# Kernel tuning notes

Measured on AMD Instinct MI355X. Metric: run time of the kernel, lower is better.

The kernel has to match this reference:

```python
import jax, jax.numpy as jnp
import numpy as np

D_MODEL = 1024
N_HEADS = 16
HEAD = D_MODEL // N_HEADS  # 64
D_FF = 4096
LN_EPS = 1e-5


def _layernorm(x, g, b):
    mu = jnp.mean(x, axis=-1, keepdims=True)
    var = jnp.mean(jnp.square(x - mu), axis=-1, keepdims=True)
    return (x - mu) * jax.lax.rsqrt(var + LN_EPS) * g + b


def _mha(q_in, k_in, v_in, Wq, Wk, Wv, bv, causal):
    # Wq/Wk/Wv: [H, d_model, head]; bv: [H, head] (value proj has bias, q/k do not)
    q = jnp.einsum('bsd,hde->bhse', q_in, Wq)
    k = jnp.einsum('btd,hde->bhte', k_in, Wk)
    v = jnp.einsum('btd,hde->bhte', v_in, Wv) + bv[None, :, None, :]
    scale = HEAD ** -0.5
    scores = jnp.einsum('bhse,bhte->bhst', q, k) * scale
    if causal:
        S, T = scores.shape[-2], scores.shape[-1]
        mask = jnp.tril(jnp.ones((S, T), dtype=bool))
        scores = jnp.where(mask, scores, -jnp.inf)
    p = jax.nn.softmax(scores, axis=-1)
    o = jnp.einsum('bhst,bhte->bhse', p, v)  # [B,H,S,head]
    B, H, S, E = o.shape
    return o.transpose(0, 2, 1, 3).reshape(B, S, H * E)  # concat heads in order


def setup_inputs() -> dict:
    key = jax.random.key(0)
    ks = jax.random.split(key, 20)
    B, S, T = 2, 2048, 2048
    sd = D_MODEL ** -0.5
    inp = {
        'input_tensor': jax.random.normal(ks[0], (B, S, D_MODEL), jnp.float32),
        'encoder_output': jax.random.normal(ks[1], (B, T, D_MODEL), jnp.float32),
        # masked self-attention params
        'Wq1': jax.random.normal(ks[2], (N_HEADS, D_MODEL, HEAD), jnp.float32) * sd,
        'Wk1': jax.random.normal(ks[3], (N_HEADS, D_MODEL, HEAD), jnp.float32) * sd,
        'Wv1': jax.random.normal(ks[4], (N_HEADS, D_MODEL, HEAD), jnp.float32) * sd,
        'bv1': jnp.zeros((N_HEADS, HEAD), jnp.float32),
        # cross-attention params
        'Wq2': jax.random.normal(ks[5], (N_HEADS, D_MODEL, HEAD), jnp.float32) * sd,
        'Wk2': jax.random.normal(ks[6], (N_HEADS, D_MODEL, HEAD), jnp.float32) * sd,
        'Wv2': jax.random.normal(ks[7], (N_HEADS, D_MODEL, HEAD), jnp.float32) * sd,
        'bv2': jnp.zeros((N_HEADS, HEAD), jnp.float32),
        # layernorms
        'g1': jnp.ones((D_MODEL,), jnp.float32), 'be1': jnp.zeros((D_MODEL,), jnp.float32),
        'g2': jnp.ones((D_MODEL,), jnp.float32), 'be2': jnp.zeros((D_MODEL,), jnp.float32),
        'g3': jnp.ones((D_MODEL,), jnp.float32), 'be3': jnp.zeros((D_MODEL,), jnp.float32),
        # FFN
        'Wf1': jax.random.normal(ks[8], (D_MODEL, D_FF), jnp.float32) * sd,
        'bf1': jnp.zeros((D_FF,), jnp.float32),
        'Wf2': jax.random.normal(ks[9], (D_FF, D_MODEL), jnp.float32) * (D_FF ** -0.5),
        'bf2': jnp.zeros((D_MODEL,), jnp.float32),
    }
    return inp


def reference(input_tensor, encoder_output, Wq1, Wk1, Wv1, bv1, Wq2, Wk2, Wv2, bv2,
              g1, be1, g2, be2, g3, be3, Wf1, bf1, Wf2, bf2):
    x = input_tensor
    # masked (causal) self-attention; dropout is identity in eval
    sa = _mha(x, x, x, Wq1, Wk1, Wv1, bv1, causal=True)
    x = _layernorm(sa + input_tensor, g1, be1)
    # cross-attention with encoder output (no mask)
    ca = _mha(x, encoder_output, encoder_output, Wq2, Wk2, Wv2, bv2, causal=False)
    x = _layernorm(x + ca, g2, be2)
    # FFN
    ffn = jax.nn.relu(x @ Wf1 + bf1) @ Wf2 + bf2
    x = _layernorm(x + ffn, g3, be3)
    return x
```

## Files before the change

### kernel.cpp

```cpp
#include <hip/hip_runtime.h>
#include <stdint.h>
#include <stddef.h>

typedef __attribute__((ext_vector_type(8))) short short8;
typedef __attribute__((ext_vector_type(4))) short short4_t;
typedef __attribute__((ext_vector_type(4))) float float4_t;
typedef __attribute__((ext_vector_type(4))) unsigned uint4_t;

#define DEV static __device__ __forceinline__

#define QSCALE 0.18033688011112042f

DEV short f2bf(float f) {
  unsigned u = __builtin_bit_cast(unsigned, f);
  u = (u + 0x7FFFu + ((u >> 16) & 1u)) >> 16;
  return (short)(unsigned short)u;
}

DEV void load_lds16(const short* g, short* l) {
  __builtin_amdgcn_global_load_lds((const __attribute__((address_space(1))) void*)g,
                                   (__attribute__((address_space(3))) void*)l,
                                   16, 0, 0);
}

__global__ __launch_bounds__(256) void transpose_cvt(const float* __restrict__ src,
                                                     short* __restrict__ dst,
                                                     int R, int C) {
  __shared__ float t[64][65];
  src += (size_t)blockIdx.z * R * C;
  dst += (size_t)blockIdx.z * R * C;
  const int tid = threadIdx.x;
  const int r0 = blockIdx.y * 64, c0 = blockIdx.x * 64;
#pragma unroll
  for (int i = 0; i < 16; i++) {
    int r = i * 4 + (tid >> 6);
    t[r][tid & 63] = src[(size_t)(r0 + r) * C + c0 + (tid & 63)];
  }
  __syncthreads();
#pragma unroll
  for (int i = 0; i < 16; i++) {
    int c = i * 4 + (tid >> 6);
    dst[(size_t)(c0 + c) * R + r0 + (tid & 63)] = f2bf(t[tid & 63][c]);
  }
}

struct Repack6 {
  const float* src[6];
  short* dst[6];
};
__global__ __launch_bounds__(256) void transpose_cvt6(Repack6 a) {
  __shared__ float t[64][65];
  const int mat = blockIdx.z >> 4;
  const int head = blockIdx.z & 15;
  const float* src = a.src[mat] + (size_t)head * 1024 * 64;
  short* dst = a.dst[mat] + (size_t)head * 64 * 1024;
  const int tid = threadIdx.x;
  const int r0 = blockIdx.y * 64;
#pragma unroll
  for (int i = 0; i < 16; i++) {
    int r = i * 4 + (tid >> 6);
    t[r][tid & 63] = src[(size_t)(r0 + r) * 64 + (tid & 63)];
  }
  __syncthreads();
#pragma unroll
  for (int i = 0; i < 16; i++) {
    int c = i * 4 + (tid >> 6);
    dst[(size_t)c * 1024 + r0 + (tid & 63)] = f2bf(t[tid & 63][c]);
  }
}

__global__ __launch_bounds__(256) void cvt_bf16_2(const float* __restrict__ inA,
                                                  short* __restrict__ outA,
                                                  const float* __restrict__ inB,
                                                  short* __restrict__ outB, int n4) {
  int i = blockIdx.x * 256 + threadIdx.x;
  const float* in = blockIdx.z ? inB : inA;
  short* out = blockIdx.z ? outB : outA;
  if (i < n4) {
    float4_t v = ((const float4_t*)in)[i];
    short4_t o;
    o.x = f2bf(v.x); o.y = f2bf(v.y); o.z = f2bf(v.z); o.w = f2bf(v.w);
    ((short4_t*)out)[i] = o;
  }
}

struct GemmArgs {
  const short* A;
  const short* Bt;
  int M, N, K;
  float* outf;
  short* outb;
  short* Qo;
  short* Ko;
  short* Vt;
  const float* bias;
};

template <int MODE>
DEV void scatter1(const GemmArgs& args, int row, int col, float v) {
  if constexpr (MODE == 0) {
    int sel = col >> 10, cc = col & 1023;
    int h = cc >> 6, e = cc & 63;
    int b_ = row >> 11, s = row & 2047;
    if (sel == 0)
      args.Qo[(((size_t)(b_ * 16 + h)) * 2048 + s) * 64 + e] = f2bf(v * QSCALE);
    else if (sel == 1)
      args.Ko[(((size_t)(b_ * 16 + h)) * 2048 + s) * 64 + e] = f2bf(v);
    else {
      v += args.bias[cc];
      args.Vt[(((size_t)(b_ * 16 + h)) * 64 + e) * 2048 + s] = f2bf(v);
    }
  } else if constexpr (MODE == 1) {
    int h = col >> 6, e = col & 63;
    int b_ = row >> 11, s = row & 2047;
    args.Qo[(((size_t)(b_ * 16 + h)) * 2048 + s) * 64 + e] = f2bf(v * QSCALE);
  } else if constexpr (MODE == 2) {
    int sel = col >> 10, cc = col & 1023;
    int h = cc >> 6, e = cc & 63;
    int b_ = row >> 11, s = row & 2047;
    if (sel == 0)
      args.Ko[(((size_t)(b_ * 16 + h)) * 2048 + s) * 64 + e] = f2bf(v);
    else {
      v += args.bias[cc];
      args.Vt[(((size_t)(b_ * 16 + h)) * 64 + e) * 2048 + s] = f2bf(v);
    }
  } else if constexpr (MODE == 3) {
    v += args.bias[col];
    v = v > 0.f ? v : 0.f;
    args.outb[(size_t)row * args.N + col] = f2bf(v);
  } else {
    v += args.bias[col];
    args.outf[(size_t)row * args.N + col] = v;
  }
}

template <int MODE>
__global__ __launch_bounds__(256) void gemm_k(GemmArgs args) {
  constexpr int BM = 128, BK = 64;
  __shared__ short As[2][BM * BK];
  __shared__ short Bs[2][BM * BK];
  const int tid = threadIdx.x;
  const int lane = tid & 63;
  const int w = tid >> 6;
  const int wr = w >> 1, wc = w & 1;

  const int nwgx = gridDim.x;
  const int nxy = nwgx * gridDim.y;
  const int nwg = nxy * gridDim.z;
  const int orig = (blockIdx.z * gridDim.y + blockIdx.y) * nwgx + blockIdx.x;
  const int q8 = nwg >> 3;
  const int swz = (orig & 7) * q8 + (orig >> 3);
  const int zsl = swz / nxy;
  const int xy = swz % nxy;
  const int row0 = (xy / nwgx) * BM;
  const int col0 = (xy % nwgx) * BM;

  const int K = args.K;
  const int kLen = K / gridDim.z;
  const int kbase = zsl * kLen;
  const short* Ab = args.A + (size_t)row0 * K;
  const short* Bb = args.Bt + (size_t)col0 * K;
  float4_t acc[4][4] = {};
  const int r = lane & 15, kg = lane >> 4, rx = r & 7;

  auto stage = [&](int buf, int k0) {
#pragma unroll
    for (int i = 0; i < 4; i++) {
      int c = i * 256 + tid;
      int rw = c >> 3, sc = (c & 7) ^ (rw & 7);
      load_lds16(Ab + (size_t)rw * K + k0 + sc * 8, &As[buf][c * 8]);
    }
#pragma unroll
    for (int i = 0; i < 4; i++) {
      int c = i * 256 + tid;
      int rw = c >> 3, sc = (c & 7) ^ (rw & 7);
      load_lds16(Bb + (size_t)rw * K + k0 + sc * 8, &Bs[buf][c * 8]);
    }
  };

  stage(0, kbase);
  __syncthreads();
  int buf = 0;
  const int nk = kLen / BK;
  for (int t = 0; t < nk; t++) {
    if (t + 1 < nk) stage(buf ^ 1, kbase + (t + 1) * BK);
#pragma unroll
    for (int kk = 0; kk < BK; kk += 32) {
      const int ch = kk >> 3;
      short8 a[4], b[4];
#pragma unroll
      for (int m = 0; m < 4; m++)
        a[m] = *(const short8*)&As[buf][(wr * 64 + m * 16 + r) * BK + ((ch + kg) ^ rx) * 8];
#pragma unroll
      for (int n = 0; n < 4; n++)
        b[n] = *(const short8*)&Bs[buf][(wc * 64 + n * 16 + r) * BK + ((ch + kg) ^ rx) * 8];
#pragma unroll
      for (int m = 0; m < 4; m++)
#pragma unroll
        for (int n = 0; n < 4; n++)
          acc[m][n] = __builtin_amdgcn_mfma_f32_16x16x32_bf16(a[m], b[n], acc[m][n], 0, 0, 0);
    }
    __syncthreads();
    buf ^= 1;
  }

  float* dst5 = args.outf + (size_t)zsl * args.M * args.N;
#pragma unroll
  for (int m = 0; m < 4; m++)
#pragma unroll
    for (int n = 0; n < 4; n++)
#pragma unroll
      for (int j = 0; j < 4; j++) {
        int row = row0 + wr * 64 + m * 16 + kg * 4 + j;
        int col = col0 + wc * 64 + n * 16 + r;
        if constexpr (MODE == 5)
          dst5[(size_t)row * args.N + col] = acc[m][n][j];
        else
          scatter1<MODE>(args, row, col, acc[m][n][j]);
      }
}

template <int MODE>
__global__ __launch_bounds__(512, 2) void gemm256_k(GemmArgs args) {
  extern __shared__ short lds[];
  const int tid = threadIdx.x;
  const int lane = tid & 63;
  const int w = tid >> 6;
  const int wr = w >> 2, wc = w & 3;

  const int nwgx = gridDim.x;
  const int nwg = nwgx * gridDim.y;
  const int orig = blockIdx.y * nwgx + blockIdx.x;
  const int q8 = nwg >> 3;
  const int swz = (orig & 7) * q8 + (orig >> 3);
  const int row0 = (swz / nwgx) * 256;
  const int col0 = (swz % nwgx) * 256;

  const int K = args.K;
  const short* Ab = args.A + (size_t)row0 * K;
  const short* Bb = args.Bt + (size_t)col0 * K;
  const int r = lane & 15, kg = lane >> 4, rx = r & 7;
  float4_t acc[8][4] = {};

  auto stage = [&](int buf, int k0) {
    short* Ad = lds + buf * 16384;
    short* Bd = lds + 32768 + buf * 16384;
#pragma unroll
    for (int i = 0; i < 4; i++) {
      int c = i * 512 + tid;
      int rw = c >> 3, sc = (c & 7) ^ (rw & 7);
      load_lds16(Ab + (size_t)rw * K + k0 + sc * 8, Ad + c * 8);
    }
#pragma unroll
    for (int i = 0; i < 4; i++) {
      int c = i * 512 + tid;
      int rw = c >> 3, sc = (c & 7) ^ (rw & 7);
      load_lds16(Bb + (size_t)rw * K + k0 + sc * 8, Bd + c * 8);
    }
  };

  stage(0, 0);
  __syncthreads();
  int buf = 0;
  const int nk = K / 64;
  for (int t = 0; t < nk; t++) {
    if (t + 1 < nk) stage(buf ^ 1, (t + 1) * 64);
    const short* Ar = lds + buf * 16384;
    const short* Br = lds + 32768 + buf * 16384;
#pragma unroll
    for (int kk = 0; kk < 64; kk += 32) {
      const int ch = kk >> 3;
      short8 a[8], b[4];
#pragma unroll
      for (int m = 0; m < 8; m++)
        a[m] = *(const short8*)&Ar[(wr * 128 + m * 16 + r) * 64 + ((ch + kg) ^ rx) * 8];
#pragma unroll
      for (int n = 0; n < 4; n++)
        b[n] = *(const short8*)&Br[(wc * 64 + n * 16 + r) * 64 + ((ch + kg) ^ rx) * 8];
#pragma unroll
      for (int m = 0; m < 8; m++)
#pragma unroll
        for (int n = 0; n < 4; n++)
          acc[m][n] = __builtin_amdgcn_mfma_f32_16x16x32_bf16(a[m], b[n], acc[m][n], 0, 0, 0);
    }
    __syncthreads();
    buf ^= 1;
  }

#pragma unroll
  for (int m = 0; m < 8; m++)
#pragma unroll
    for (int n = 0; n < 4; n++)
#pragma unroll
      for (int j = 0; j < 4; j++)
        scatter1<MODE>(args, row0 + wr * 128 + m * 16 + kg * 4 + j,
                       col0 + wc * 64 + n * 16 + r, acc[m][n][j]);
}

template <bool CAUSAL>
__global__ __launch_bounds__(256) void attn_k(const short* __restrict__ Q,
                                              const short* __restrict__ Kq,
                                              const short* __restrict__ Vt,
                                              float* __restrict__ Out) {
  __shared__ short kst[2][64 * 64];
  __shared__ short vst[2][64 * 64];
  __shared__ unsigned p_lds[4][16 * 32];
  const int tid = threadIdx.x;
  const int lane = tid & 63;
  const int w = tid >> 6;
  const int bh = blockIdx.y;
  const int b_ = bh >> 4, h = bh & 15;
  const int qt = (blockIdx.x + blockIdx.y) & (gridDim.x - 1);
  const int q0 = qt * 64 + w * 16;
  const int r = lane & 15, kg = lane >> 4;
  const int rx = r & 7;
  const size_t base = (size_t)bh * 2048 * 64;
  const short* Qb = Q + base;
  const short* Kb = Kq + base;
  const short* Vb = Vt + base;

  short8 q[2];
#pragma unroll
  for (int half = 0; half < 2; half++)
    q[half] = *(const short8*)&Qb[(size_t)(q0 + r) * 64 + half * 32 + kg * 8];

  float4_t o[4] = {};
  float lp = 0.f;

  const int NT = CAUSAL ? qt + 1 : 32;
  const float4_t zero4 = {0.f, 0.f, 0.f, 0.f};

  const int c0 = tid, c1 = tid + 256;
  const int row0s = c0 >> 3, cc0 = (c0 & 7) ^ (row0s & 7);
  const int row1s = c1 >> 3, cc1 = (c1 & 7) ^ (row1s & 7);

  auto stage = [&](int buf, int kt) {
    const short* ktk = Kb + (size_t)kt * 64 * 64;
    const short* ktv = Vb + (size_t)kt * 64;
    load_lds16(ktk + row0s * 64 + cc0 * 8, &kst[buf][c0 * 8]);
    load_lds16(ktk + row1s * 64 + cc1 * 8, &kst[buf][c1 * 8]);
    load_lds16(ktv + (size_t)row0s * 2048 + cc0 * 8, &vst[buf][c0 * 8]);
    load_lds16(ktv + (size_t)row1s * 2048 + cc1 * 8, &vst[buf][c1 * 8]);
  };

  stage(0, 0);
  __syncthreads();
  int buf = 0;

  for (int kt = 0; kt < NT; kt++) {
    if (kt + 1 < NT) stage(buf ^ 1, kt + 1);

    short8 kb[4][2];
#pragma unroll
    for (int grp = 0; grp < 4; grp++)
#pragma unroll
      for (int half = 0; half < 2; half++)
        kb[grp][half] = *(const short8*)&kst[buf][(grp * 16 + r) * 64 + ((half * 4 + kg) ^ rx) * 8];

    float4_t sc[4];
    __builtin_amdgcn_s_setprio(1);
#pragma unroll
    for (int grp = 0; grp < 4; grp++) {
      float4_t t0 = __builtin_amdgcn_mfma_f32_16x16x32_bf16(kb[grp][0], q[0], zero4, 0, 0, 0);
      sc[grp] = __builtin_amdgcn_mfma_f32_16x16x32_bf16(kb[grp][1], q[1], t0, 0, 0, 0);
    }
    __builtin_amdgcn_s_setprio(0);

    float s[16];
#pragma unroll
    for (int grp = 0; grp < 4; grp++)
#pragma unroll
      for (int j = 0; j < 4; j++) s[grp * 4 + j] = sc[grp][j];

    if (CAUSAL && kt == NT - 1) {
      const int qrow = q0 + r;
#pragma unroll
      for (int grp = 0; grp < 4; grp++)
#pragma unroll
        for (int j = 0; j < 4; j++)
          if (kt * 64 + grp * 16 + kg * 4 + j > qrow) s[grp * 4 + j] = -1e30f;
    }

    float p[16];
    float ps = 0.f;
#pragma unroll
    for (int i = 0; i < 16; i++) {
      p[i] = __builtin_amdgcn_exp2f(s[i]);
      ps += p[i];
    }
    lp += ps;

    unsigned* p32 = &p_lds[w][0];
#pragma unroll
    for (int grp = 0; grp < 4; grp++) {
      unsigned pk01, pk23;
      asm("v_cvt_pk_bf16_f32 %0, %1, %2" : "=v"(pk01) : "v"(p[grp * 4 + 0]), "v"(p[grp * 4 + 1]));
      asm("v_cvt_pk_bf16_f32 %0, %1, %2" : "=v"(pk23) : "v"(p[grp * 4 + 2]), "v"(p[grp * 4 + 3]));
      int idx = r * 32 + ((2 * grp + (kg >> 1)) ^ rx) * 4 + (kg & 1) * 2;
      p32[idx] = pk01;
      p32[idx + 1] = pk23;
    }
    __builtin_amdgcn_sched_barrier(0);

    short8 pa[2];
#pragma unroll
    for (int half = 0; half < 2; half++) {
      const int db = r * 32 + ((half * 4 + kg) ^ rx) * 4;
      uint4_t t;
      t.x = p32[db + 0];
      t.y = p32[db + 1];
      t.z = p32[db + 2];
      t.w = p32[db + 3];
      pa[half] = __builtin_bit_cast(short8, t);
    }

    __builtin_amdgcn_s_setprio(1);
#pragma unroll
    for (int n = 0; n < 4; n++) {
      short8 v0 = *(const short8*)&vst[buf][(n * 16 + r) * 64 + ((0 * 4 + kg) ^ rx) * 8];
      short8 v1 = *(const short8*)&vst[buf][(n * 16 + r) * 64 + ((1 * 4 + kg) ^ rx) * 8];
      o[n] = __builtin_amdgcn_mfma_f32_16x16x32_bf16(v0, pa[0], o[n], 0, 0, 0);
      o[n] = __builtin_amdgcn_mfma_f32_16x16x32_bf16(v1, pa[1], o[n], 0, 0, 0);
    }
    __builtin_amdgcn_s_setprio(0);

    __syncthreads();
    buf ^= 1;
  }

  lp += __shfl_xor(lp, 16);
  lp += __shfl_xor(lp, 32);
  const float inv = 1.0f / lp;
  float* orow = Out + ((size_t)b_ * 2048 + q0 + r) * 1024 + h * 64;
#pragma unroll
  for (int n = 0; n < 4; n++)
#pragma unroll
    for (int j = 0; j < 4; j++)
      orow[n * 16 + kg * 4 + j] = o[n][j] * inv;
}

__global__ __launch_bounds__(256) void add_ln_k(const float* __restrict__ X,
                                                const float* __restrict__ Y,
                                                const float* __restrict__ g,
                                                const float* __restrict__ be,
                                                float* __restrict__ outf,
                                                short* __restrict__ outb) {
  __shared__ float red[8];
  const int row = blockIdx.x;
  const int t = threadIdx.x;
  const int lane = t & 63, w = t >> 6;
  float4_t v = ((const float4_t*)(X + (size_t)row * 1024))[t];
  float4_t u = ((const float4_t*)(Y + (size_t)row * 1024))[t];
  v.x += u.x; v.y += u.y; v.z += u.z; v.w += u.w;
  float s = v.x + v.y + v.z + v.w;
#pragma unroll
  for (int off = 32; off >= 1; off >>= 1) s += __shfl_xor(s, off);
  if (lane == 0) red[w] = s;
  __syncthreads();
  float mean = (red[0] + red[1] + red[2] + red[3]) * (1.f / 1024.f);
  float dx = v.x - mean, dy = v.y - mean, dz = v.z - mean, dw = v.w - mean;
  float q2 = dx * dx + dy * dy + dz * dz + dw * dw;
#pragma unroll
  for (int off = 32; off >= 1; off >>= 1) q2 += __shfl_xor(q2, off);
  if (lane == 0) red[4 + w] = q2;
  __syncthreads();
  float var = (red[4] + red[5] + red[6] + red[7]) * (1.f / 1024.f);
  float rs = rsqrtf(var + 1e-5f);
  float4_t gg = ((const float4_t*)g)[t];
  float4_t bb = ((const float4_t*)be)[t];
  float4_t o;
  o.x = dx * rs * gg.x + bb.x;
  o.y = dy * rs * gg.y + bb.y;
  o.z = dz * rs * gg.z + bb.z;
  o.w = dw * rs * gg.w + bb.w;
  ((float4_t*)(outf + (size_t)row * 1024))[t] = o;
  if (outb != nullptr) {
    short4_t ob;
    ob.x = f2bf(o.x); ob.y = f2bf(o.y); ob.z = f2bf(o.z); ob.w = f2bf(o.w);
    ((short4_t*)(outb + (size_t)row * 1024))[t] = ob;
  }
}

__global__ __launch_bounds__(256) void add_ln2_k(const float* __restrict__ X,
                                                 const float* __restrict__ P0,
                                                 const float* __restrict__ P1,
                                                 const float* __restrict__ bias,
                                                 const float* __restrict__ g,
                                                 const float* __restrict__ be,
                                                 float* __restrict__ outf) {
  __shared__ float red[8];
  const int row = blockIdx.x;
  const int t = threadIdx.x;
  const int lane = t & 63, w = t >> 6;
  float4_t v = ((const float4_t*)(X + (size_t)row * 1024))[t];
  float4_t u0 = ((const float4_t*)(P0 + (size_t)row * 1024))[t];
  float4_t u1 = ((const float4_t*)(P1 + (size_t)row * 1024))[t];
  float4_t bi = ((const float4_t*)bias)[t];
  v.x += u0.x + u1.x + bi.x;
  v.y += u0.y + u1.y + bi.y;
  v.z += u0.z + u1.z + bi.z;
  v.w += u0.w + u1.w + bi.w;
  float s = v.x + v.y + v.z + v.w;
#pragma unroll
  for (int off = 32; off >= 1; off >>= 1) s += __shfl_xor(s, off);
  if (lane == 0) red[w] = s;
  __syncthreads();
  float mean = (red[0] + red[1] + red[2] + red[3]) * (1.f / 1024.f);
  float dx = v.x - mean, dy = v.y - mean, dz = v.z - mean, dw = v.w - mean;
  float q2 = dx * dx + dy * dy + dz * dz + dw * dw;
#pragma unroll
  for (int off = 32; off >= 1; off >>= 1) q2 += __shfl_xor(q2, off);
  if (lane == 0) red[4 + w] = q2;
  __syncthreads();
  float var = (red[4] + red[5] + red[6] + red[7]) * (1.f / 1024.f);
  float rs = rsqrtf(var + 1e-5f);
  float4_t gg = ((const float4_t*)g)[t];
  float4_t bb = ((const float4_t*)be)[t];
  float4_t o;
  o.x = dx * rs * gg.x + bb.x;
  o.y = dy * rs * gg.y + bb.y;
  o.z = dz * rs * gg.z + bb.z;
  o.w = dw * rs * gg.w + bb.w;
  ((float4_t*)(outf + (size_t)row * 1024))[t] = o;
}

extern "C" void kernel_launch(void* const* d_in, const int* in_sizes, int n_in,
                              void* d_out, int out_size, void* d_ws, size_t ws_size,
                              hipStream_t stream) {
  (void)in_sizes; (void)n_in; (void)out_size; (void)ws_size;
  const float* x_in = (const float*)d_in[0];
  const float* enc  = (const float*)d_in[1];
  const float* Wq1  = (const float*)d_in[2];
  const float* Wk1  = (const float*)d_in[3];
  const float* Wv1  = (const float*)d_in[4];
  const float* bv1  = (const float*)d_in[5];
  const float* Wq2  = (const float*)d_in[6];
  const float* Wk2  = (const float*)d_in[7];
  const float* Wv2  = (const float*)d_in[8];
  const float* bv2  = (const float*)d_in[9];
  const float* g1   = (const float*)d_in[10];
  const float* be1  = (const float*)d_in[11];
  const float* g2   = (const float*)d_in[12];
  const float* be2  = (const float*)d_in[13];
  const float* g3   = (const float*)d_in[14];
  const float* be3  = (const float*)d_in[15];
  const float* Wf1  = (const float*)d_in[16];
  const float* bf1  = (const float*)d_in[17];
  const float* Wf2  = (const float*)d_in[18];
  const float* bf2  = (const float*)d_in[19];
  float* out = (float*)d_out;

  (void)hipFuncSetAttribute((const void*)gemm256_k<0>,
                            hipFuncAttributeMaxDynamicSharedMemorySize, 131072);
  (void)hipFuncSetAttribute((const void*)gemm256_k<3>,
                            hipFuncAttributeMaxDynamicSharedMemorySize, 131072);

  char* ws = (char*)d_ws;
  size_t off = 0;
  auto alloc = [&](size_t bytes) -> void* {
    void* p = ws + off;
    off += (bytes + 255) & ~(size_t)255;
    return p;
  };
  short* wqkv1t = (short*)alloc((size_t)3072 * 1024 * 2);
  short* wq2t   = (short*)alloc((size_t)1024 * 1024 * 2);
  short* wkv2t  = (short*)alloc((size_t)2048 * 1024 * 2);
  short* wf1t   = (short*)alloc((size_t)4096 * 1024 * 2);
  short* wf2t   = (short*)alloc((size_t)1024 * 4096 * 2);
  short* act_bf = (short*)alloc((size_t)4096 * 1024 * 2);
  short* enc_bf = (short*)alloc((size_t)4096 * 1024 * 2);
  short* Qb     = (short*)alloc((size_t)4096 * 1024 * 2);
  short* Kb     = (short*)alloc((size_t)4096 * 1024 * 2);
  short* Vtb    = (short*)alloc((size_t)4096 * 1024 * 2);
  float* tmp_f  = (float*)alloc((size_t)4096 * 1024 * 4);
  float* xbuf   = (float*)alloc((size_t)4096 * 1024 * 4);
  short* h_bf   = (short*)alloc((size_t)4096 * 4096 * 2);
  float* pbuf   = (float*)alloc((size_t)2 * 4096 * 1024 * 4);

  dim3 blk(256);
  dim3 blk5(512);
  Repack6 rp;
  rp.src[0] = Wq1; rp.dst[0] = wqkv1t;
  rp.src[1] = Wk1; rp.dst[1] = wqkv1t + 1024 * 1024;
  rp.src[2] = Wv1; rp.dst[2] = wqkv1t + 2 * 1024 * 1024;
  rp.src[3] = Wq2; rp.dst[3] = wq2t;
  rp.src[4] = Wk2; rp.dst[4] = wkv2t;
  rp.src[5] = Wv2; rp.dst[5] = wkv2t + 1024 * 1024;
  transpose_cvt6<<<dim3(1, 16, 96), blk, 0, stream>>>(rp);
  transpose_cvt<<<dim3(64, 16, 1), blk, 0, stream>>>(Wf1, wf1t, 1024, 4096);
  transpose_cvt<<<dim3(16, 64, 1), blk, 0, stream>>>(Wf2, wf2t, 4096, 1024);
  cvt_bf16_2<<<dim3(4096, 1, 2), blk, 0, stream>>>(x_in, act_bf, enc, enc_bf, 1048576);

  GemmArgs ga;
  ga.A = act_bf; ga.Bt = wqkv1t; ga.M = 4096; ga.N = 3072; ga.K = 1024;
  ga.outf = nullptr; ga.outb = nullptr; ga.Qo = Qb; ga.Ko = Kb; ga.Vt = Vtb; ga.bias = bv1;
  gemm256_k<0><<<dim3(12, 16), blk5, 131072, stream>>>(ga);
  attn_k<true><<<dim3(32, 32), blk, 0, stream>>>(Qb, Kb, Vtb, tmp_f);
  add_ln_k<<<4096, blk, 0, stream>>>(tmp_f, x_in, g1, be1, xbuf, act_bf);

  ga.A = act_bf; ga.Bt = wq2t; ga.M = 4096; ga.N = 1024; ga.K = 1024;
  ga.Qo = Qb; ga.Ko = nullptr; ga.Vt = nullptr; ga.bias = nullptr;
  gemm_k<1><<<dim3(8, 32), blk, 0, stream>>>(ga);
  ga.A = enc_bf; ga.Bt = wkv2t; ga.M = 4096; ga.N = 2048; ga.K = 1024;
  ga.Qo = nullptr; ga.Ko = Kb; ga.Vt = Vtb; ga.bias = bv2;
  gemm_k<2><<<dim3(16, 32), blk, 0, stream>>>(ga);
  attn_k<false><<<dim3(32, 32), blk, 0, stream>>>(Qb, Kb, Vtb, tmp_f);
  add_ln_k<<<4096, blk, 0, stream>>>(xbuf, tmp_f, g2, be2, xbuf, act_bf);

  ga.A = act_bf; ga.Bt = wf1t; ga.M = 4096; ga.N = 4096; ga.K = 1024;
  ga.outb = h_bf; ga.bias = bf1; ga.Qo = nullptr; ga.Ko = nullptr; ga.Vt = nullptr;
  gemm256_k<3><<<dim3(16, 16), blk5, 131072, stream>>>(ga);
  ga.A = h_bf; ga.Bt = wf2t; ga.M = 4096; ga.N = 1024; ga.K = 4096;
  ga.outf = pbuf; ga.outb = nullptr; ga.bias = nullptr;
  gemm_k<5><<<dim3(8, 32, 2), blk, 0, stream>>>(ga);
  add_ln2_k<<<4096, blk, 0, stream>>>(xbuf, pbuf, pbuf + (size_t)4096 * 1024,
                                      bf2, g3, be3, out);
}
```

Baseline: 346.7 us.

## Merge cross-attention Q and KV projection GEMMs into one launch; unroll attention double-buffer

The separate Q-projection and KV-projection GEMMs for cross-attention are combined into a single grouped kernel that assigns the first 256 swizzled workgroups to the Q projection and the remaining 512 to the K/V projection. This cuts one launch and lets the two small GEMMs share the GPU instead of running back to back with tail underutilization. Separately, the attention loop is unrolled by two with compile-time buffer indices, so LDS addresses are constant and the runtime buffer toggle goes away. The risks are divergent scatter paths inside the fused kernel and more code size in the attention kernel.

```diff
diff --git a/kernel.cpp b/kernel.cpp
--- a/kernel.cpp
+++ b/kernel.cpp
@@ -1,6 +1,7 @@
 #include <hip/hip_runtime.h>
 #include <stdint.h>
 #include <stddef.h>
+#include <type_traits>
 
 typedef __attribute__((ext_vector_type(8))) short short8;
 typedef __attribute__((ext_vector_type(4))) short short4_t;
@@ -217,6 +218,86 @@
           dst5[(size_t)row * args.N + col] = acc[m][n][j];
         else
           scatter1<MODE>(args, row, col, acc[m][n][j]);
+      }
+}
+
+__global__ __launch_bounds__(256) void gemm_dual_k(GemmArgs a1, GemmArgs a2) {
+  constexpr int BM = 128, BK = 64;
+  __shared__ short As[2][BM * BK];
+  __shared__ short Bs[2][BM * BK];
+  const int tid = threadIdx.x;
+  const int lane = tid & 63;
+  const int w = tid >> 6;
+  const int wr = w >> 1, wc = w & 1;
+
+  const int nwg = gridDim.x;
+  const int orig = blockIdx.x;
+  const int q8 = nwg >> 3;
+  const int swz = (orig & 7) * q8 + (orig >> 3);
+  const bool isA = swz < 256;
+  const GemmArgs& args = isA ? a1 : a2;
+  const int id = isA ? swz : swz - 256;
+  const int ncols = isA ? 8 : 16;
+  const int row0 = (id / ncols) * BM;
+  const int col0 = (id % ncols) * BM;
+
+  const int K = 1024;
+  const short* Ab = args.A + (size_t)row0 * K;
+  const short* Bb = args.Bt + (size_t)col0 * K;
+  float4_t acc[4][4] = {};
+  const int r = lane & 15, kg = lane >> 4, rx = r & 7;
+
+  auto stage = [&](int buf, int k0) {
+#pragma unroll
+    for (int i = 0; i < 4; i++) {
+      int c = i * 256 + tid;
+      int rw = c >> 3, sc = (c & 7) ^ (rw & 7);
+      load_lds16(Ab + (size_t)rw * K + k0 + sc * 8, &As[buf][c * 8]);
+    }
+#pragma unroll
+    for (int i = 0; i < 4; i++) {
+      int c = i * 256 + tid;
+      int rw = c >> 3, sc = (c & 7) ^ (rw & 7);
+      load_lds16(Bb + (size_t)rw * K + k0 + sc * 8, &Bs[buf][c * 8]);
+    }
+  };
+
+  stage(0, 0);
+  __syncthreads();
+  int buf = 0;
+  const int nk = K / BK;
+  for (int t = 0; t < nk; t++) {
+    if (t + 1 < nk) stage(buf ^ 1, (t + 1) * BK);
+#pragma unroll
+    for (int kk = 0; kk < BK; kk += 32) {
+      const int ch = kk >> 3;
+      short8 a[4], b[4];
+#pragma unroll
+      for (int m = 0; m < 4; m++)
+        a[m] = *(const short8*)&As[buf][(wr * 64 + m * 16 + r) * BK + ((ch + kg) ^ rx) * 8];
+#pragma unroll
+      for (int n = 0; n < 4; n++)
+        b[n] = *(const short8*)&Bs[buf][(wc * 64 + n * 16 + r) * BK + ((ch + kg) ^ rx) * 8];
+#pragma unroll
+      for (int m = 0; m < 4; m++)
+#pragma unroll
+        for (int n = 0; n < 4; n++)
+          acc[m][n] = __builtin_amdgcn_mfma_f32_16x16x32_bf16(a[m], b[n], acc[m][n], 0, 0, 0);
+    }
+    __syncthreads();
+    buf ^= 1;
+  }
+
+#pragma unroll
+  for (int m = 0; m < 4; m++)
+#pragma unroll
+    for (int n = 0; n < 4; n++)
+#pragma unroll
+      for (int j = 0; j < 4; j++) {
+        int row = row0 + wr * 64 + m * 16 + kg * 4 + j;
+        int col = col0 + wc * 64 + n * 16 + r;
+        if (isA) scatter1<1>(args, row, col, acc[m][n][j]);
+        else     scatter1<2>(args, row, col, acc[m][n][j]);
       }
 }
 
@@ -343,19 +424,14 @@
     load_lds16(ktv + (size_t)row1s * 2048 + cc1 * 8, &vst[buf][c1 * 8]);
   };
 
-  stage(0, 0);
-  __syncthreads();
-  int buf = 0;
-
-  for (int kt = 0; kt < NT; kt++) {
-    if (kt + 1 < NT) stage(buf ^ 1, kt + 1);
-
+  auto body = [&](auto BUFC, int kt) {
+    constexpr int BUF = decltype(BUFC)::value;
     short8 kb[4][2];
 #pragma unroll
     for (int grp = 0; grp < 4; grp++)
 #pragma unroll
       for (int half = 0; half < 2; half++)
-        kb[grp][half] = *(const short8*)&kst[buf][(grp * 16 + r) * 64 + ((half * 4 + kg) ^ rx) * 8];
+        kb[grp][half] = *(const short8*)&kst[BUF][(grp * 16 + r) * 64 + ((half * 4 + kg) ^ rx) * 8];
 
     float4_t sc[4];
     __builtin_amdgcn_s_setprio(1);
@@ -417,15 +493,25 @@
     __builtin_amdgcn_s_setprio(1);
 #pragma unroll
     for (int n = 0; n < 4; n++) {
-      short8 v0 = *(const short8*)&vst[buf][(n * 16 + r) * 64 + ((0 * 4 + kg) ^ rx) * 8];
-      short8 v1 = *(const short8*)&vst[buf][(n * 16 + r) * 64 + ((1 * 4 + kg) ^ rx) * 8];
+      short8 v0 = *(const short8*)&vst[BUF][(n * 16 + r) * 64 + ((0 * 4 + kg) ^ rx) * 8];
+      short8 v1 = *(const short8*)&vst[BUF][(n * 16 + r) * 64 + ((1 * 4 + kg) ^ rx) * 8];
       o[n] = __builtin_amdgcn_mfma_f32_16x16x32_bf16(v0, pa[0], o[n], 0, 0, 0);
       o[n] = __builtin_amdgcn_mfma_f32_16x16x32_bf16(v1, pa[1], o[n], 0, 0, 0);
     }
     __builtin_amdgcn_s_setprio(0);
-
+  };
+
+  stage(0, 0);
+  __syncthreads();
+
+  for (int kt = 0; kt < NT; kt += 2) {
+    if (kt + 1 < NT) stage(1, kt + 1);
+    body(std::integral_constant<int, 0>{}, kt);
     __syncthreads();
-    buf ^= 1;
+    if (kt + 1 >= NT) break;
+    if (kt + 2 < NT) stage(0, kt + 2);
+    body(std::integral_constant<int, 1>{}, kt + 1);
+    __syncthreads();
   }
 
   lp += __shfl_xor(lp, 16);
@@ -598,12 +684,12 @@
   attn_k<true><<<dim3(32, 32), blk, 0, stream>>>(Qb, Kb, Vtb, tmp_f);
   add_ln_k<<<4096, blk, 0, stream>>>(tmp_f, x_in, g1, be1, xbuf, act_bf);
 
-  ga.A = act_bf; ga.Bt = wq2t; ga.M = 4096; ga.N = 1024; ga.K = 1024;
-  ga.Qo = Qb; ga.Ko = nullptr; ga.Vt = nullptr; ga.bias = nullptr;
-  gemm_k<1><<<dim3(8, 32), blk, 0, stream>>>(ga);
-  ga.A = enc_bf; ga.Bt = wkv2t; ga.M = 4096; ga.N = 2048; ga.K = 1024;
-  ga.Qo = nullptr; ga.Ko = Kb; ga.Vt = Vtb; ga.bias = bv2;
-  gemm_k<2><<<dim3(16, 32), blk, 0, stream>>>(ga);
+  GemmArgs gq, gkv;
+  gq.A = act_bf; gq.Bt = wq2t; gq.M = 4096; gq.N = 1024; gq.K = 1024;
+  gq.outf = nullptr; gq.outb = nullptr; gq.Qo = Qb; gq.Ko = nullptr; gq.Vt = nullptr; gq.bias = nullptr;
+  gkv.A = enc_bf; gkv.Bt = wkv2t; gkv.M = 4096; gkv.N = 2048; gkv.K = 1024;
+  gkv.outf = nullptr; gkv.outb = nullptr; gkv.Qo = nullptr; gkv.Ko = Kb; gkv.Vt = Vtb; gkv.bias = bv2;
+  gemm_dual_k<<<dim3(768), blk, 0, stream>>>(gq, gkv);
   attn_k<false><<<dim3(32, 32), blk, 0, stream>>>(Qb, Kb, Vtb, tmp_f);
   add_ln_k<<<4096, blk, 0, stream>>>(xbuf, tmp_f, g2, be2, xbuf, act_bf);
 
```

New measurement: 353.6 us. No clear change (+2.0%).
